# Performance work log

Hardware: AMD Instinct MI355X
Metric: run time of the kernel (lower is better)

Reference implementation:

```python
import jax, jax.numpy as jnp
import numpy as np

N = 50000        # num nodes
E = 800000       # num edges (before self-loops)
IN = 256         # in_channels
HID = 32         # hidden_channels per head
HEADS = 8
OUT = 64         # out_channels (layer 2, heads=1)
NEG_SLOPE = 0.2  # PyG GATConv default leaky_relu slope


def setup_inputs() -> dict:
    key = jax.random.key(0)
    ks = jax.random.split(key, 12)
    def rn(k, shape, scale=0.1):
        return jax.random.normal(k, shape, dtype=jnp.float32) * scale
    x = jax.random.normal(ks[0], (N, IN), dtype=jnp.float32)
    edge_index = jax.random.randint(ks[1], (2, E), 0, N, dtype=jnp.int64)
    return {
        "x": x,
        "edge_index": edge_index,
        # GATConv 1: in=256 -> 32 per head, 8 heads, concat
        "W1": rn(ks[2], (IN, HEADS * HID)),
        "att_src1": rn(ks[3], (HEADS, HID)),
        "att_dst1": rn(ks[4], (HEADS, HID)),
        "b1": jnp.zeros((HEADS * HID,), jnp.float32),
        # GATConv 2: in=256 -> 64, 1 head
        "W2": rn(ks[5], (HEADS * HID, OUT)),
        "att_src2": rn(ks[6], (1, OUT)),
        "att_dst2": rn(ks[7], (1, OUT)),
        "b2": jnp.zeros((OUT,), jnp.float32),
    }


def _gat_conv(x, src, dst, W, att_src, att_dst, bias, heads, out_ch):
    """PyG-style GATConv (add_self_loops already applied to src/dst).
    x: [N, F_in]; src/dst: [E']; returns [N, heads*out_ch] (concat)."""
    n = x.shape[0]
    h = (x @ W).reshape(n, heads, out_ch)                     # [N,H,F]
    a_src = jnp.einsum('nhf,hf->nh', h, att_src)              # [N,H]
    a_dst = jnp.einsum('nhf,hf->nh', h, att_dst)
    e = jax.nn.leaky_relu(a_src[src] + a_dst[dst], NEG_SLOPE)  # [E',H]
    # scatter-softmax over incoming edges of each dst node
    m = jax.ops.segment_max(e, dst, num_segments=n)            # [N,H]
    ex = jnp.exp(e - m[dst])
    denom = jax.ops.segment_sum(ex, dst, num_segments=n)       # [N,H]
    alpha = ex / denom[dst]                                    # [E',H]
    msg = alpha[:, :, None] * h[src]                           # [E',H,F]
    out = jax.ops.segment_sum(msg, dst, num_segments=n)        # [N,H,F]
    return out.reshape(n, heads * out_ch) + bias


def reference(x, edge_index, W1, att_src1, att_dst1, b1, W2, att_src2, att_dst2, b2):
    n = x.shape[0]
    loop = jnp.arange(n, dtype=edge_index.dtype)
    src = jnp.concatenate([edge_index[0], loop])  # add self-loops (PyG default)
    dst = jnp.concatenate([edge_index[1], loop])
    h = _gat_conv(x, src, dst, W1, att_src1, att_dst1, b1, HEADS, HID)
    h = jax.nn.relu(h)
    out = _gat_conv(h, src, dst, W2, att_src2, att_dst2, b2, 1, OUT)
    return out
```

## Files before the change

### kernel.cpp

```cpp
#include <hip/hip_runtime.h>
#include <hip/hip_bf16.h>


#define HEADS 8
#define HID 32
#define F1 256
#define F2 64
#define NEG_SLOPE 0.2f
#define CAP 128

typedef __attribute__((ext_vector_type(8))) short bf16x8;
typedef __attribute__((ext_vector_type(4))) float f32x4;
typedef __attribute__((ext_vector_type(8))) unsigned short u16x8;

__device__ __forceinline__ unsigned short f2b(float f) {
    union { float f; unsigned int i; } x; x.f = f;
    unsigned int r = x.i + 0x7fffu + ((x.i >> 16) & 1u);
    return (unsigned short)(r >> 16);
}
__device__ __forceinline__ float b2f(unsigned short u) {
    union { unsigned int i; float f; } x; x.i = ((unsigned int)u) << 16;
    return x.f;
}
__device__ __forceinline__ float leaky(float v) {
    return v > 0.f ? v : NEG_SLOPE * v;
}

__global__ void setup_kernel(const float* __restrict__ W1,
                             const float* __restrict__ W2,
                             unsigned short* __restrict__ W1T,
                             unsigned short* __restrict__ W2T,
                             int* __restrict__ cursor,
                             unsigned short* __restrict__ h1b,
                             unsigned short* __restrict__ h2b,
                             float* __restrict__ a_src8,
                             float* __restrict__ a_src2, int Nn) {
    const int i = blockIdx.x * 256 + threadIdx.x;
    const int T1 = F1 * F1;
    const int T2 = T1 + F1 * F2;
    const int T3 = T2 + Nn;
    const int T4 = T3 + F1;
    const int T5 = T4 + F2;
    const int T6 = T5 + 8;
    const int T7 = T6 + 1;
    if (i < T1) {
        const int k = i >> 8, n = i & (F1 - 1);
        W1T[(size_t)n * F1 + k] = f2b(W1[i]);
    } else if (i < T2) {
        const int j = i - T1;
        const int k = j >> 6, n = j & (F2 - 1);
        W2T[(size_t)n * F1 + k] = f2b(W2[j]);
    } else if (i < T3) {
        cursor[i - T2] = 0;
    } else if (i < T4) {
        h1b[(size_t)Nn * F1 + (i - T3)] = 0;
    } else if (i < T5) {
        h2b[(size_t)Nn * F2 + (i - T4)] = 0;
    } else if (i < T6) {
        a_src8[(size_t)Nn * 8 + (i - T5)] = -1e30f;
    } else if (i < T7) {
        a_src2[Nn] = -1e30f;
    }
}

__global__ void scatter_kernel(const int* __restrict__ ei, int E,
                               int* __restrict__ cursor,
                               int* __restrict__ bucket) {
    const int e = blockIdx.x * blockDim.x + threadIdx.x;
    if (e >= E) return;
    const int d = ei[E + e];
    const int pos = atomicAdd(&cursor[d], 1);
    if (pos < CAP) bucket[(size_t)d * CAP + pos] = ei[e];
}

__global__ void pad_kernel(const int* __restrict__ cursor,
                           int* __restrict__ bucket, int Nn) {
    const int d = blockIdx.x * 256 + threadIdx.x;
    if (d >= Nn) return;
    const int c0 = min(cursor[d], CAP);
    const int ce = min((c0 + 7) & ~7, CAP);
    for (int i = c0; i < ce; ++i) bucket[(size_t)d * CAP + i] = Nn;
}

template<int BN, bool A_FP32, int OUT_MODE>
__global__ __launch_bounds__(256) void mfma_gemm(
        const void* __restrict__ A,
        const unsigned short* __restrict__ BT,
        void* __restrict__ C, int M, int N, int K) {
    constexpr int BM = 128, BK = 32;
    __shared__ unsigned short As[BM * BK];
    __shared__ unsigned short Bs[BN * BK];
    const int tid = threadIdx.x;
    const int wave = tid >> 6, lane = tid & 63;
    const int quad = lane >> 4, l16 = lane & 15;
    const int brow = blockIdx.x * BM;
    const int bcol = blockIdx.y * BN;

    constexpr int MI = (BN == 128) ? 4 : 2;
    constexpr int NJ = 4;
    const int wm = (BN == 128) ? (wave & 1) * 64 : wave * 32;
    const int wn = (BN == 128) ? (wave >> 1) * 64 : 0;

    f32x4 acc[MI][NJ] = {};

    for (int k0 = 0; k0 < K; k0 += BK) {
#pragma unroll
        for (int it = 0; it < (BM * BK) / (256 * 8); ++it) {
            const int idx = it * 256 + tid;
            const int r = idx >> 2;
            const int kk = (idx & 3) * 8;
            const int gr = brow + r;
            if (A_FP32) {
                const float* Af = (const float*)A;
                float4 a0 = make_float4(0.f, 0.f, 0.f, 0.f);
                float4 a1 = make_float4(0.f, 0.f, 0.f, 0.f);
                if (gr < M) {
                    a0 = *(const float4*)&Af[(size_t)gr * K + k0 + kk];
                    a1 = *(const float4*)&Af[(size_t)gr * K + k0 + kk + 4];
                }
                ushort4 lo, hi;
                lo.x = f2b(a0.x); lo.y = f2b(a0.y); lo.z = f2b(a0.z); lo.w = f2b(a0.w);
                hi.x = f2b(a1.x); hi.y = f2b(a1.y); hi.z = f2b(a1.z); hi.w = f2b(a1.w);
                *(ushort4*)&As[r * BK + kk] = lo;
                *(ushort4*)&As[r * BK + kk + 4] = hi;
            } else {
                const unsigned short* Ab = (const unsigned short*)A;
                uint4 v = make_uint4(0u, 0u, 0u, 0u);
                if (gr < M) v = *(const uint4*)&Ab[(size_t)gr * K + k0 + kk];
                *(uint4*)&As[r * BK + kk] = v;
            }
        }
#pragma unroll
        for (int it = 0; it < (BN * BK) / (256 * 8); ++it) {
            const int idx = it * 256 + tid;
            const int r = idx >> 2;
            const int kk = (idx & 3) * 8;
            const uint4 v = *(const uint4*)&BT[(size_t)(bcol + r) * K + k0 + kk];
            *(uint4*)&Bs[r * BK + kk] = v;
        }
        __syncthreads();
        bf16x8 af[MI], bfr[NJ];
#pragma unroll
        for (int i = 0; i < MI; ++i)
            af[i] = *(const bf16x8*)&As[(wm + i * 16 + l16) * BK + quad * 8];
#pragma unroll
        for (int j = 0; j < NJ; ++j)
            bfr[j] = *(const bf16x8*)&Bs[(wn + j * 16 + l16) * BK + quad * 8];
#pragma unroll
        for (int i = 0; i < MI; ++i)
#pragma unroll
            for (int j = 0; j < NJ; ++j)
                acc[i][j] = __builtin_amdgcn_mfma_f32_16x16x32_bf16(
                    af[i], bfr[j], acc[i][j], 0, 0, 0);
        __syncthreads();
    }
#pragma unroll
    for (int i = 0; i < MI; ++i) {
#pragma unroll
        for (int r = 0; r < 4; ++r) {
            const int row = brow + wm + i * 16 + quad * 4 + r;
            if (row >= M) continue;
#pragma unroll
            for (int j = 0; j < NJ; ++j) {
                const int col = bcol + wn + j * 16 + l16;
                const float v = acc[i][j][r];
                if (OUT_MODE == 0) {
                    ((float*)C)[(size_t)row * N + col] = v;
                } else {
                    ((unsigned short*)C)[(size_t)row * N + col] = f2b(v);
                }
            }
        }
    }
}

__global__ void att1n_kernel(const unsigned short* __restrict__ h1b,
                             const float* __restrict__ att_src,
                             const float* __restrict__ att_dst,
                             float* __restrict__ a_src8,
                             float* __restrict__ a_dst8, int Nn) {
    const int idx = blockIdx.x * 256 + threadIdx.x;
    const int n = idx >> 3, h = idx & 7;
    if (n >= Nn) return;
    const unsigned short* hp = h1b + (size_t)n * F1 + h * HID;
    const float* as = att_src + h * HID;
    const float* ad = att_dst + h * HID;
    float s = 0.f, dd = 0.f;
#pragma unroll
    for (int f = 0; f < HID; ++f) {
        const float v = b2f(hp[f]);
        s += v * as[f];
        dd += v * ad[f];
    }
    a_src8[(size_t)n * 8 + h] = s;
    a_dst8[(size_t)n * 8 + h] = dd;
}

__global__ void att2_kernel(const unsigned short* __restrict__ h2b,
                            const float* __restrict__ att_src,
                            const float* __restrict__ att_dst,
                            float* __restrict__ a_src,
                            float* __restrict__ a_dst, int Nn) {
    const int n = blockIdx.x * blockDim.x + threadIdx.x;
    if (n >= Nn) return;
    const unsigned short* hp = h2b + (size_t)n * F2;
    float s = 0.f, d = 0.f;
#pragma unroll
    for (int f = 0; f < F2; ++f) {
        const float v = b2f(hp[f]);
        s += v * att_src[f];
        d += v * att_dst[f];
    }
    a_src[n] = s;
    a_dst[n] = d;
}

__global__ __launch_bounds__(256, 4) void gather1_kernel(
        const int* __restrict__ cursor, const int* __restrict__ bucket,
        const float* __restrict__ a_src8, const float* __restrict__ a_dst8,
        const unsigned short* __restrict__ h1b, const float* __restrict__ b1,
        unsigned short* __restrict__ out1b, int Nn) {
    const int lane = threadIdx.x & 63;
    const int wv   = threadIdx.x >> 6;
    const int slot = lane >> 5;
    const int l    = lane & 31;
    const int hd   = l >> 2;
    const int d = blockIdx.x * 8 + wv * 2 + slot;
    if (d >= Nn) return;

    const float adst = a_dst8[(size_t)d * 8 + hd];

    float denom, acc[8];
    {
        const float w = __expf(leaky(a_src8[(size_t)d * 8 + hd] + adst));
        const u16x8 v = *(const u16x8*)&h1b[(size_t)d * F1 + l * 8];
        denom = w;
#pragma unroll
        for (int q = 0; q < 8; ++q) acc[q] = w * b2f(v[q]);
    }
    const int base = d * CAP;
    const int cnt = min(cursor[d], CAP);
    const int cntp = (cnt + 7) & ~7;
    for (int i = 0; i < cntp; i += 8) {
        const int4 sa = *(const int4*)&bucket[base + i];
        const int4 sb = *(const int4*)&bucket[base + i + 4];
        int s[8] = { sa.x, sa.y, sa.z, sa.w, sb.x, sb.y, sb.z, sb.w };
        float e[8];
#pragma unroll
        for (int j = 0; j < 8; ++j) e[j] = a_src8[(size_t)s[j] * 8 + hd];
        u16x8 vv[8];
#pragma unroll
        for (int j = 0; j < 8; ++j)
            vv[j] = *(const u16x8*)&h1b[(size_t)s[j] * F1 + l * 8];
#pragma unroll
        for (int j = 0; j < 8; ++j) {
            const float w = __expf(leaky(e[j] + adst));
            denom += w;
#pragma unroll
            for (int q = 0; q < 8; ++q) acc[q] += w * b2f(vv[j][q]);
        }
    }
    const float inv = 1.f / denom;
    const int c = l * 8;
    const float4 bv0 = *(const float4*)&b1[c];
    const float4 bv1 = *(const float4*)&b1[c + 4];
    u16x8 o;
    o[0] = f2b(fmaxf(acc[0] * inv + bv0.x, 0.f));
    o[1] = f2b(fmaxf(acc[1] * inv + bv0.y, 0.f));
    o[2] = f2b(fmaxf(acc[2] * inv + bv0.z, 0.f));
    o[3] = f2b(fmaxf(acc[3] * inv + bv0.w, 0.f));
    o[4] = f2b(fmaxf(acc[4] * inv + bv1.x, 0.f));
    o[5] = f2b(fmaxf(acc[5] * inv + bv1.y, 0.f));
    o[6] = f2b(fmaxf(acc[6] * inv + bv1.z, 0.f));
    o[7] = f2b(fmaxf(acc[7] * inv + bv1.w, 0.f));
    *(u16x8*)&out1b[(size_t)d * F1 + c] = o;
}

__global__ __launch_bounds__(256, 4) void gather2_kernel(
        const int* __restrict__ cursor, const int* __restrict__ bucket,
        const float* __restrict__ a_src, const float* __restrict__ a_dst,
        const unsigned short* __restrict__ h2b, const float* __restrict__ b2,
        float* __restrict__ out, int Nn) {
    const int lane = threadIdx.x & 63;
    const int slot = lane >> 4;
    const int l    = lane & 15;
    const int d = blockIdx.x * 16 + (threadIdx.x >> 6) * 4 + slot;
    if (d >= Nn) return;
    const int c = l * 4;

    const float adst = a_dst[d];
    float a0, a1, a2, a3, denom;
    {
        const float w = __expf(leaky(a_src[d] + adst));
        const ushort4 v = *(const ushort4*)&h2b[(size_t)d * F2 + c];
        denom = w;
        a0 = w * b2f(v.x); a1 = w * b2f(v.y);
        a2 = w * b2f(v.z); a3 = w * b2f(v.w);
    }
    const int base = d * CAP;
    const int cnt = min(cursor[d], CAP);
    const int cntp = (cnt + 7) & ~7;
    for (int i = 0; i < cntp; i += 8) {
        const int4 sa = *(const int4*)&bucket[base + i];
        const int4 sb = *(const int4*)&bucket[base + i + 4];
        int s[8] = { sa.x, sa.y, sa.z, sa.w, sb.x, sb.y, sb.z, sb.w };
        float e[8];
        ushort4 vv[8];
#pragma unroll
        for (int jj = 0; jj < 8; ++jj) {
            e[jj] = a_src[s[jj]];
            vv[jj] = *(const ushort4*)&h2b[(size_t)s[jj] * F2 + c];
        }
#pragma unroll
        for (int jj = 0; jj < 8; ++jj) {
            const float w = __expf(leaky(e[jj] + adst));
            denom += w;
            a0 += w * b2f(vv[jj].x); a1 += w * b2f(vv[jj].y);
            a2 += w * b2f(vv[jj].z); a3 += w * b2f(vv[jj].w);
        }
    }
    const float inv = 1.f / denom;
    float4 o;
    o.x = a0 * inv + b2[c + 0];
    o.y = a1 * inv + b2[c + 1];
    o.z = a2 * inv + b2[c + 2];
    o.w = a3 * inv + b2[c + 3];
    *(float4*)&out[(size_t)d * F2 + c] = o;
}

extern "C" void kernel_launch(void* const* d_in, const int* in_sizes, int n_in,
                              void* d_out, int out_size, void* d_ws, size_t ws_size,
                              hipStream_t stream) {
    const float* x        = (const float*)d_in[0];
    const int*   ei       = (const int*)d_in[1];
    const float* W1       = (const float*)d_in[2];
    const float* att_src1 = (const float*)d_in[3];
    const float* att_dst1 = (const float*)d_in[4];
    const float* b1       = (const float*)d_in[5];
    const float* W2       = (const float*)d_in[6];
    const float* att_src2 = (const float*)d_in[7];
    const float* att_dst2 = (const float*)d_in[8];
    const float* b2       = (const float*)d_in[9];
    float* out = (float*)d_out;

    const int Nn = in_sizes[0] / F1;
    const int E  = in_sizes[1] / 2;

    char* p = (char*)d_ws;
    unsigned short* h1b   = (unsigned short*)p; p += (size_t)(Nn + 1) * F1 * 2;
    unsigned short* out1b = (unsigned short*)p; p += (size_t)Nn * F1 * 2;
    unsigned short* W1T   = (unsigned short*)p; p += (size_t)F1 * F1 * 2;
    unsigned short* W2T   = (unsigned short*)p; p += (size_t)F2 * F1 * 2;
    unsigned short* h2b   = (unsigned short*)p; p += (size_t)(Nn + 1) * F2 * 2;
    float* a_src8 = (float*)p; p += (size_t)(Nn + 1) * 8 * 4;
    float* a_dst8 = (float*)p; p += (size_t)Nn * 8 * 4;
    float* a_src2 = (float*)p; p += (size_t)(Nn + 4) * 4;
    float* a_dst2 = (float*)p; p += (size_t)Nn * 4;
    int* cursor  = (int*)p; p += (size_t)Nn * 4;
    int* bucket  = (int*)p; p += (size_t)Nn * CAP * 4;

    {
        const int total = F1 * F1 + F1 * F2 + Nn + F1 + F2 + 8 + 1;
        setup_kernel<<<(total + 255) / 256, 256, 0, stream>>>(
            W1, W2, W1T, W2T, cursor, h1b, h2b, a_src8, a_src2, Nn);
    }
    scatter_kernel<<<(E + 255) / 256, 256, 0, stream>>>(ei, E, cursor, bucket);
    pad_kernel<<<(Nn + 255) / 256, 256, 0, stream>>>(cursor, bucket, Nn);

    {
        dim3 grid((Nn + 127) / 128, F1 / 128);
        mfma_gemm<128, true, 1><<<grid, 256, 0, stream>>>(
            x, W1T, h1b, Nn, F1, F1);
    }
    att1n_kernel<<<(Nn * 8 + 255) / 256, 256, 0, stream>>>(
        h1b, att_src1, att_dst1, a_src8, a_dst8, Nn);
    gather1_kernel<<<(Nn + 7) / 8, 256, 0, stream>>>(
        cursor, bucket, a_src8, a_dst8, h1b, b1, out1b, Nn);

    {
        dim3 grid((Nn + 127) / 128, F2 / 64);
        mfma_gemm<64, false, 1><<<grid, 256, 0, stream>>>(
            out1b, W2T, h2b, Nn, F2, F1);
    }
    att2_kernel<<<(Nn + 255) / 256, 256, 0, stream>>>(
        h2b, att_src2, att_dst2, a_src2, a_dst2, Nn);
    gather2_kernel<<<(Nn + 15) / 16, 256, 0, stream>>>(
        cursor, bucket, a_src2, a_dst2, h2b, b2, out, Nn);
}
```

Measured before the change: 291.0 us.

## Store layer-1 features head-major and gather per head for cache locality

Layer-1 projected features and attention scores are now stored head-major ([head][node][32]), written that way by the GEMM epilogue. The gather kernel is regrouped so each block handles one head across 64 destination nodes, with 4 lanes per node. Each head's slice of features (about 3.2MB) can then stay in cache during the random neighbour gathers. Nontemporal loads and stores are also added for the bucket and output streams. The cost is that each bucket list is read once per head, eight times in total, and the GEMM output stores become more scattered.

```diff
diff --git a/kernel.cpp b/kernel.cpp
--- a/kernel.cpp
+++ b/kernel.cpp
@@ -12,6 +12,7 @@
 typedef __attribute__((ext_vector_type(8))) short bf16x8;
 typedef __attribute__((ext_vector_type(4))) float f32x4;
 typedef __attribute__((ext_vector_type(8))) unsigned short u16x8;
+typedef __attribute__((ext_vector_type(4))) int i32x4;
 
 __device__ __forceinline__ unsigned short f2b(float f) {
     union { float f; unsigned int i; } x; x.f = f;
@@ -31,17 +32,18 @@
                              unsigned short* __restrict__ W1T,
                              unsigned short* __restrict__ W2T,
                              int* __restrict__ cursor,
-                             unsigned short* __restrict__ h1b,
+                             unsigned short* __restrict__ h1hm,
                              unsigned short* __restrict__ h2b,
-                             float* __restrict__ a_src8,
+                             float* __restrict__ a_src1,
                              float* __restrict__ a_src2, int Nn) {
     const int i = blockIdx.x * 256 + threadIdx.x;
+    const int Ns = Nn + 1;
     const int T1 = F1 * F1;
     const int T2 = T1 + F1 * F2;
     const int T3 = T2 + Nn;
-    const int T4 = T3 + F1;
+    const int T4 = T3 + HEADS * HID;
     const int T5 = T4 + F2;
-    const int T6 = T5 + 8;
+    const int T6 = T5 + HEADS;
     const int T7 = T6 + 1;
     if (i < T1) {
         const int k = i >> 8, n = i & (F1 - 1);
@@ -53,11 +55,13 @@
     } else if (i < T3) {
         cursor[i - T2] = 0;
     } else if (i < T4) {
-        h1b[(size_t)Nn * F1 + (i - T3)] = 0;
+        const int j = i - T3;
+        const int h = j >> 5, f = j & 31;
+        h1hm[((size_t)h * Ns + Nn) * HID + f] = 0;
     } else if (i < T5) {
         h2b[(size_t)Nn * F2 + (i - T4)] = 0;
     } else if (i < T6) {
-        a_src8[(size_t)Nn * 8 + (i - T5)] = -1e30f;
+        a_src1[(size_t)(i - T5) * Ns + Nn] = -1e30f;
     } else if (i < T7) {
         a_src2[Nn] = -1e30f;
     }
@@ -70,7 +74,7 @@
     if (e >= E) return;
     const int d = ei[E + e];
     const int pos = atomicAdd(&cursor[d], 1);
-    if (pos < CAP) bucket[(size_t)d * CAP + pos] = ei[e];
+    if (pos < CAP) __builtin_nontemporal_store(ei[e], &bucket[(size_t)d * CAP + pos]);
 }
 
 __global__ void pad_kernel(const int* __restrict__ cursor,
@@ -79,14 +83,15 @@
     if (d >= Nn) return;
     const int c0 = min(cursor[d], CAP);
     const int ce = min((c0 + 7) & ~7, CAP);
-    for (int i = c0; i < ce; ++i) bucket[(size_t)d * CAP + i] = Nn;
+    for (int i = c0; i < ce; ++i)
+        __builtin_nontemporal_store(Nn, &bucket[(size_t)d * CAP + i]);
 }
 
 template<int BN, bool A_FP32, int OUT_MODE>
 __global__ __launch_bounds__(256) void mfma_gemm(
         const void* __restrict__ A,
         const unsigned short* __restrict__ BT,
-        void* __restrict__ C, int M, int N, int K) {
+        void* __restrict__ C, int M, int N, int K, int Mstr) {
     constexpr int BM = 128, BK = 32;
     __shared__ unsigned short As[BM * BK];
     __shared__ unsigned short Bs[BN * BK];
@@ -164,25 +169,27 @@
             for (int j = 0; j < NJ; ++j) {
                 const int col = bcol + wn + j * 16 + l16;
                 const float v = acc[i][j][r];
-                if (OUT_MODE == 0) {
-                    ((float*)C)[(size_t)row * N + col] = v;
+                if (OUT_MODE == 1) {
+                    ((unsigned short*)C)[(size_t)row * N + col] = f2b(v);
                 } else {
-                    ((unsigned short*)C)[(size_t)row * N + col] = f2b(v);
+                    ((unsigned short*)C)[((size_t)(col >> 5) * Mstr + row) * HID
+                                         + (col & 31)] = f2b(v);
                 }
             }
         }
     }
 }
 
-__global__ void att1n_kernel(const unsigned short* __restrict__ h1b,
-                             const float* __restrict__ att_src,
-                             const float* __restrict__ att_dst,
-                             float* __restrict__ a_src8,
-                             float* __restrict__ a_dst8, int Nn) {
-    const int idx = blockIdx.x * 256 + threadIdx.x;
-    const int n = idx >> 3, h = idx & 7;
+__global__ void att1_kernel(const unsigned short* __restrict__ h1hm,
+                            const float* __restrict__ att_src,
+                            const float* __restrict__ att_dst,
+                            float* __restrict__ a_src,
+                            float* __restrict__ a_dst, int Nn) {
+    const int n = blockIdx.x * blockDim.x + threadIdx.x;
+    const int h = blockIdx.y;
     if (n >= Nn) return;
-    const unsigned short* hp = h1b + (size_t)n * F1 + h * HID;
+    const int Ns = Nn + 1;
+    const unsigned short* hp = h1hm + ((size_t)h * Ns + n) * HID;
     const float* as = att_src + h * HID;
     const float* ad = att_dst + h * HID;
     float s = 0.f, dd = 0.f;
@@ -192,8 +199,8 @@
         s += v * as[f];
         dd += v * ad[f];
     }
-    a_src8[(size_t)n * 8 + h] = s;
-    a_dst8[(size_t)n * 8 + h] = dd;
+    a_src[(size_t)h * Ns + n] = s;
+    a_dst[(size_t)h * Ns + n] = dd;
 }
 
 __global__ void att2_kernel(const unsigned short* __restrict__ h2b,
@@ -217,23 +224,26 @@
 
 __global__ __launch_bounds__(256, 4) void gather1_kernel(
         const int* __restrict__ cursor, const int* __restrict__ bucket,
-        const float* __restrict__ a_src8, const float* __restrict__ a_dst8,
-        const unsigned short* __restrict__ h1b, const float* __restrict__ b1,
+        const float* __restrict__ a_src, const float* __restrict__ a_dst,
+        const unsigned short* __restrict__ h1hm, const float* __restrict__ b1,
         unsigned short* __restrict__ out1b, int Nn) {
+    const int h = blockIdx.x & 7;
     const int lane = threadIdx.x & 63;
     const int wv   = threadIdx.x >> 6;
-    const int slot = lane >> 5;
-    const int l    = lane & 31;
-    const int hd   = l >> 2;
-    const int d = blockIdx.x * 8 + wv * 2 + slot;
+    const int slot = lane >> 2;
+    const int cl   = lane & 3;
+    const int d = (blockIdx.x >> 3) * 64 + wv * 16 + slot;
     if (d >= Nn) return;
-
-    const float adst = a_dst8[(size_t)d * 8 + hd];
+    const int Ns = Nn + 1;
+
+    const unsigned short* hh = h1hm + (size_t)h * Ns * HID;
+    const float* asrc = a_src + (size_t)h * Ns;
+    const float adst = a_dst[(size_t)h * Ns + d];
 
     float denom, acc[8];
     {
-        const float w = __expf(leaky(a_src8[(size_t)d * 8 + hd] + adst));
-        const u16x8 v = *(const u16x8*)&h1b[(size_t)d * F1 + l * 8];
+        const float w = __expf(leaky(asrc[d] + adst));
+        const u16x8 v = *(const u16x8*)&hh[(size_t)d * HID + cl * 8];
         denom = w;
 #pragma unroll
         for (int q = 0; q < 8; ++q) acc[q] = w * b2f(v[q]);
@@ -242,16 +252,16 @@
     const int cnt = min(cursor[d], CAP);
     const int cntp = (cnt + 7) & ~7;
     for (int i = 0; i < cntp; i += 8) {
-        const int4 sa = *(const int4*)&bucket[base + i];
-        const int4 sb = *(const int4*)&bucket[base + i + 4];
+        const i32x4 sa = __builtin_nontemporal_load((const i32x4*)&bucket[base + i]);
+        const i32x4 sb = __builtin_nontemporal_load((const i32x4*)&bucket[base + i + 4]);
         int s[8] = { sa.x, sa.y, sa.z, sa.w, sb.x, sb.y, sb.z, sb.w };
         float e[8];
 #pragma unroll
-        for (int j = 0; j < 8; ++j) e[j] = a_src8[(size_t)s[j] * 8 + hd];
+        for (int j = 0; j < 8; ++j) e[j] = asrc[s[j]];
         u16x8 vv[8];
 #pragma unroll
         for (int j = 0; j < 8; ++j)
-            vv[j] = *(const u16x8*)&h1b[(size_t)s[j] * F1 + l * 8];
+            vv[j] = *(const u16x8*)&hh[(size_t)s[j] * HID + cl * 8];
 #pragma unroll
         for (int j = 0; j < 8; ++j) {
             const float w = __expf(leaky(e[j] + adst));
@@ -261,7 +271,7 @@
         }
     }
     const float inv = 1.f / denom;
-    const int c = l * 8;
+    const int c = h * HID + cl * 8;
     const float4 bv0 = *(const float4*)&b1[c];
     const float4 bv1 = *(const float4*)&b1[c + 4];
     u16x8 o;
@@ -273,7 +283,7 @@
     o[5] = f2b(fmaxf(acc[5] * inv + bv1.y, 0.f));
     o[6] = f2b(fmaxf(acc[6] * inv + bv1.z, 0.f));
     o[7] = f2b(fmaxf(acc[7] * inv + bv1.w, 0.f));
-    *(u16x8*)&out1b[(size_t)d * F1 + c] = o;
+    __builtin_nontemporal_store(o, (u16x8*)&out1b[(size_t)d * F1 + c]);
 }
 
 __global__ __launch_bounds__(256, 4) void gather2_kernel(
@@ -301,8 +311,8 @@
     const int cnt = min(cursor[d], CAP);
     const int cntp = (cnt + 7) & ~7;
     for (int i = 0; i < cntp; i += 8) {
-        const int4 sa = *(const int4*)&bucket[base + i];
-        const int4 sb = *(const int4*)&bucket[base + i + 4];
+        const i32x4 sa = __builtin_nontemporal_load((const i32x4*)&bucket[base + i]);
+        const i32x4 sb = __builtin_nontemporal_load((const i32x4*)&bucket[base + i + 4]);
         int s[8] = { sa.x, sa.y, sa.z, sa.w, sb.x, sb.y, sb.z, sb.w };
         float e[8];
         ushort4 vv[8];
@@ -320,12 +330,12 @@
         }
     }
     const float inv = 1.f / denom;
-    float4 o;
+    f32x4 o;
     o.x = a0 * inv + b2[c + 0];
     o.y = a1 * inv + b2[c + 1];
     o.z = a2 * inv + b2[c + 2];
     o.w = a3 * inv + b2[c + 3];
-    *(float4*)&out[(size_t)d * F2 + c] = o;
+    __builtin_nontemporal_store(o, (f32x4*)&out[(size_t)d * F2 + c]);
 }
 
 extern "C" void kernel_launch(void* const* d_in, const int* in_sizes, int n_in,
@@ -345,42 +355,46 @@
 
     const int Nn = in_sizes[0] / F1;
     const int E  = in_sizes[1] / 2;
+    const int Ns = Nn + 1;
 
     char* p = (char*)d_ws;
-    unsigned short* h1b   = (unsigned short*)p; p += (size_t)(Nn + 1) * F1 * 2;
+    unsigned short* h1hm  = (unsigned short*)p; p += (size_t)Ns * F1 * 2;
     unsigned short* out1b = (unsigned short*)p; p += (size_t)Nn * F1 * 2;
     unsigned short* W1T   = (unsigned short*)p; p += (size_t)F1 * F1 * 2;
     unsigned short* W2T   = (unsigned short*)p; p += (size_t)F2 * F1 * 2;
-    unsigned short* h2b   = (unsigned short*)p; p += (size_t)(Nn + 1) * F2 * 2;
-    float* a_src8 = (float*)p; p += (size_t)(Nn + 1) * 8 * 4;
-    float* a_dst8 = (float*)p; p += (size_t)Nn * 8 * 4;
+    unsigned short* h2b   = (unsigned short*)p; p += (size_t)Ns * F2 * 2;
+    float* a_src1 = (float*)p; p += (size_t)HEADS * Ns * 4;
+    float* a_dst1 = (float*)p; p += (size_t)HEADS * Ns * 4;
     float* a_src2 = (float*)p; p += (size_t)(Nn + 4) * 4;
     float* a_dst2 = (float*)p; p += (size_t)Nn * 4;
     int* cursor  = (int*)p; p += (size_t)Nn * 4;
     int* bucket  = (int*)p; p += (size_t)Nn * CAP * 4;
 
     {
-        const int total = F1 * F1 + F1 * F2 + Nn + F1 + F2 + 8 + 1;
+        const int total = F1 * F1 + F1 * F2 + Nn + HEADS * HID + F2 + HEADS + 1;
         setup_kernel<<<(total + 255) / 256, 256, 0, stream>>>(
-            W1, W2, W1T, W2T, cursor, h1b, h2b, a_src8, a_src2, Nn);
+            W1, W2, W1T, W2T, cursor, h1hm, h2b, a_src1, a_src2, Nn);
     }
     scatter_kernel<<<(E + 255) / 256, 256, 0, stream>>>(ei, E, cursor, bucket);
     pad_kernel<<<(Nn + 255) / 256, 256, 0, stream>>>(cursor, bucket, Nn);
 
     {
         dim3 grid((Nn + 127) / 128, F1 / 128);
-        mfma_gemm<128, true, 1><<<grid, 256, 0, stream>>>(
-            x, W1T, h1b, Nn, F1, F1);
-    }
-    att1n_kernel<<<(Nn * 8 + 255) / 256, 256, 0, stream>>>(
-        h1b, att_src1, att_dst1, a_src8, a_dst8, Nn);
-    gather1_kernel<<<(Nn + 7) / 8, 256, 0, stream>>>(
-        cursor, bucket, a_src8, a_dst8, h1b, b1, out1b, Nn);
+        mfma_gemm<128, true, 2><<<grid, 256, 0, stream>>>(
+            x, W1T, h1hm, Nn, F1, F1, Ns);
+    }
+    {
+        dim3 grid((Nn + 255) / 256, HEADS);
+        att1_kernel<<<grid, 256, 0, stream>>>(
+            h1hm, att_src1, att_dst1, a_src1, a_dst1, Nn);
+    }
+    gather1_kernel<<<((Nn + 63) / 64) * 8, 256, 0, stream>>>(
+        cursor, bucket, a_src1, a_dst1, h1hm, b1, out1b, Nn);
 
     {
         dim3 grid((Nn + 127) / 128, F2 / 64);
         mfma_gemm<64, false, 1><<<grid, 256, 0, stream>>>(
-            out1b, W2T, h2b, Nn, F2, F1);
+            out1b, W2T, h2b, Nn, F2, F1, 0);
     }
     att2_kernel<<<(Nn + 255) / 256, 256, 0, stream>>>(
         h2b, att_src2, att_dst2, a_src2, a_dst2, Nn);
```

Result: slower. 335.8 us (+15.4%).
